# Kernel optimization log

Hardware: AMD Instinct MI355X
Metric: run time of the kernel (lower is better)

The kernel has to match this reference:

```python
import jax, jax.numpy as jnp
import numpy as np

N_NODES = 100000
N_EDGES = 1600000
IN_CH = 128
OUT_CH = 128


def setup_inputs() -> dict:
    key = jax.random.key(0)
    k1, k2, k3 = jax.random.split(key, 3)
    x = jax.random.normal(k1, (N_NODES, IN_CH), dtype=jnp.float32)
    edge_index = jax.random.randint(k2, (2, N_EDGES), 0, N_NODES, dtype=jnp.int64)
    # glorot-like init for the linear weight, stored as [in, out]
    W = jax.random.normal(k3, (IN_CH, OUT_CH), dtype=jnp.float32) * (2.0 / (IN_CH + OUT_CH)) ** 0.5
    bias = jnp.zeros((OUT_CH,), dtype=jnp.float32)
    return {"x": x, "edge_index": edge_index, "W": W, "bias": bias}


def reference(x, edge_index, W, bias):
    N = x.shape[0]
    # linear transform (bias-free, matches Linear(in, out, bias=False))
    h = x @ W  # [N, out]

    # add self loops (improved=False -> fill_value = 1.0)
    loop = jnp.arange(N, dtype=edge_index.dtype)
    src = jnp.concatenate([edge_index[0], loop])
    dst = jnp.concatenate([edge_index[1], loop])
    ew = jnp.ones(src.shape[0], dtype=h.dtype)  # edge_weight None -> ones

    # symmetric GCN normalization: deg from dst, norm = d^-1/2[src] * w * d^-1/2[dst]
    deg = jax.ops.segment_sum(ew, dst, num_segments=N)
    deg_inv_sqrt = jnp.where(deg > 0, jax.lax.rsqrt(deg), 0.0)
    w = deg_inv_sqrt[src] * ew * deg_inv_sqrt[dst]

    # spmm aggregation: out[dst] += w * h[src]
    out = jax.ops.segment_sum(h[src] * w[:, None], dst, num_segments=N)
    return out + bias
```

## Files before the change

kernel.cpp:

```cpp
#include <hip/hip_runtime.h>
#include <hip/hip_bf16.h>

constexpr int kNodes = 100000;
constexpr int kEdges = 1600000;
constexpr int kCh    = 128;
constexpr int kCap   = 32;
constexpr int kOvfCap = 8192;
constexpr int kPartSize = kNodes / 8;
constexpr int kFillBlocks = 512;
constexpr int kGemmBlocks = (kNodes + 127) / 128;

typedef __attribute__((ext_vector_type(8))) short short8;
typedef __attribute__((ext_vector_type(4))) float floatx4;
typedef __attribute__((ext_vector_type(4))) int   intx4;


__global__ __launch_bounds__(512) void k_fused(const float* __restrict__ x,
                                               const float* __restrict__ W,
                                               const int* __restrict__ srcArr,
                                               const int* __restrict__ dstArr,
                                               int* __restrict__ cnt,
                                               int* __restrict__ bucket,
                                               int* __restrict__ ovfCnt,
                                               int* __restrict__ ovfD,
                                               int* __restrict__ ovfS,
                                               __hip_bfloat16* __restrict__ hs) {
  if (blockIdx.x < kFillBlocks) {
    int part = blockIdx.x & 7;
    int bip  = blockIdx.x >> 3;
    int lo = part * kPartSize;
    const intx4* d4 = (const intx4*)dstArr;
    const intx4* s4 = (const intx4*)srcArr;
    for (int i = bip * 512 + (int)threadIdx.x; i < kEdges / 4; i += (kFillBlocks >> 3) * 512) {
      intx4 dv = __builtin_nontemporal_load(d4 + i);
      intx4 sv = __builtin_nontemporal_load(s4 + i);
      #pragma unroll
      for (int k = 0; k < 4; k++) {
        int d = dv[k];
        if ((unsigned)(d - lo) < (unsigned)kPartSize) {
          int pos = atomicAdd(&cnt[d], 1);
          if (pos < kCap) {
            bucket[(long)d * kCap + pos] = sv[k];
          } else {
            int o = atomicAdd(ovfCnt, 1);
            if (o < kOvfCap) { ovfD[o] = d; ovfS[o] = sv[k]; }
          }
        }
      }
    }
    return;
  }

  __shared__ short8 Bf[2048];
  for (int e = threadIdx.x; e < 2048; e += 512) {
    int lane = e & 63, c = (e >> 6) & 3, tt = e >> 8;
    int quad = lane >> 4, mcol = lane & 15;
    short8 v;
    #pragma unroll
    for (int j = 0; j < 8; j++) {
      __hip_bfloat16 h = __float2bfloat16(W[(c * 32 + quad * 8 + j) * kCh + tt * 16 + mcol]);
      v[j] = *(short*)&h;
    }
    Bf[e] = v;
  }
  __syncthreads();

  int wave = threadIdx.x >> 6;
  int lane = threadIdx.x & 63;
  int quad = lane >> 4;
  int mcol = lane & 15;
  int gb = blockIdx.x - kFillBlocks;
  long rowBase = ((long)gb * 8 + wave) * 16;
  if (rowBase >= kNodes) return;

  long arow = rowBase + mcol;
  if (arow >= kNodes) arow = kNodes - 1;
  const float* xp = x + arow * kCh;
  short8 afrag[4];
  #pragma unroll
  for (int c = 0; c < 4; c++) {
    const floatx4* p = (const floatx4*)(xp + c * 32 + quad * 8);
    floatx4 v0 = __builtin_nontemporal_load(p);
    floatx4 v1 = __builtin_nontemporal_load(p + 1);
    #pragma unroll
    for (int j = 0; j < 4; j++) {
      __hip_bfloat16 h0 = __float2bfloat16(v0[j]);
      __hip_bfloat16 h1 = __float2bfloat16(v1[j]);
      afrag[c][j]     = *(short*)&h0;
      afrag[c][j + 4] = *(short*)&h1;
    }
  }

  #pragma unroll
  for (int t = 0; t < 8; t++) {
    floatx4 acc = {0.f, 0.f, 0.f, 0.f};
    #pragma unroll
    for (int c = 0; c < 4; c++) {
      short8 b = Bf[(t * 4 + c) * 64 + lane];
      acc = __builtin_amdgcn_mfma_f32_16x16x32_bf16(afrag[c], b, acc, 0, 0, 0);
    }
    #pragma unroll
    for (int i = 0; i < 4; i++) {
      long r = rowBase + quad * 4 + i;
      if (r < kNodes) {
        __hip_bfloat16 h = __float2bfloat16(acc[i]);
        __builtin_nontemporal_store(*(short*)&h, (short*)hs + r * kCh + t * 16 + mcol);
      }
    }
  }
}


__global__ __launch_bounds__(256) void k_dinv(const int* __restrict__ cnt,
                                              float* __restrict__ dinv) {
  int i = blockIdx.x * 256 + threadIdx.x;
  if (i < kNodes) dinv[i] = rsqrtf((float)(cnt[i] + 1));
}


__global__ __launch_bounds__(256) void k_aggregate(const int* __restrict__ cnt,
                                                   const int* __restrict__ bucket,
                                                   const float* __restrict__ dinv,
                                                   const int* __restrict__ ovfCnt,
                                                   const int* __restrict__ ovfD,
                                                   const int* __restrict__ ovfS,
                                                   const __hip_bfloat16* __restrict__ hs,
                                                   const float* __restrict__ bias,
                                                   float* __restrict__ out) {
  int gid  = blockIdx.x * 256 + threadIdx.x;
  int node = gid >> 6;
  int lane = gid & 63;
  if (node >= kNodes) return;

  const __hip_bfloat162* hbase = (const __hip_bfloat162*)hs;

  int degRaw = cnt[node];
  float dd = dinv[node];

  float2 sf = __bfloat1622float2(hbase[(long)node * (kCh / 2) + lane]);
  float acc0 = dd * sf.x;
  float acc1 = dd * sf.y;

  int c = degRaw < kCap ? degRaw : kCap;
  const int* bkt = bucket + (long)node * kCap;

  int j = 0;
  for (; j + 7 < c; j += 8) {
    int s[8];
    #pragma unroll
    for (int u = 0; u < 8; u++) s[u] = bkt[j + u];
    float dv[8];
    #pragma unroll
    for (int u = 0; u < 8; u++) dv[u] = dinv[s[u]];
    __hip_bfloat162 v[8];
    #pragma unroll
    for (int u = 0; u < 8; u++) v[u] = hbase[(long)s[u] * (kCh / 2) + lane];
    #pragma unroll
    for (int u = 0; u < 8; u++) {
      float2 f = __bfloat1622float2(v[u]);
      acc0 = fmaf(dv[u], f.x, acc0);
      acc1 = fmaf(dv[u], f.y, acc1);
    }
  }
  for (; j < c; ++j) {
    int s = bkt[j];
    float dv = dinv[s];
    float2 f = __bfloat1622float2(hbase[(long)s * (kCh / 2) + lane]);
    acc0 = fmaf(dv, f.x, acc0);
    acc1 = fmaf(dv, f.y, acc1);
  }

  if (degRaw > kCap) {
    int n = *ovfCnt;
    if (n > kOvfCap) n = kOvfCap;
    for (int i = 0; i < n; i++) {
      if (ovfD[i] == node) {
        int s = ovfS[i];
        float2 f = __bfloat1622float2(hbase[(long)s * (kCh / 2) + lane]);
        acc0 = fmaf(dinv[s], f.x, acc0);
        acc1 = fmaf(dinv[s], f.y, acc1);
      }
    }
  }

  float2 b = ((const float2*)bias)[lane];
  float2 o;
  o.x = dd * acc0 + b.x;
  o.y = dd * acc1 + b.y;
  ((float2*)(out + (long)node * kCh))[lane] = o;
}


extern "C" void kernel_launch(void* const* d_in, const int* in_sizes, int n_in,
                              void* d_out, int out_size, void* d_ws, size_t ws_size,
                              hipStream_t stream) {
  const float* x    = (const float*)d_in[0];
  const int*   ei   = (const int*)d_in[1];
  const float* W    = (const float*)d_in[2];
  const float* bias = (const float*)d_in[3];
  float* out = (float*)d_out;

  const int* srcArr = ei;
  const int* dstArr = ei + kEdges;

  char* ws = (char*)d_ws;
  size_t off = 0;
  __hip_bfloat16* hs = (__hip_bfloat16*)(ws + off); off += (size_t)kNodes * kCh * 2;
  int*   bucket  = (int*)  (ws + off); off += (size_t)kNodes * kCap * 4;
  float* dinv    = (float*)(ws + off); off += (size_t)kNodes * 4;
  char* zbase = ws + off;
  int*   cnt     = (int*)(ws + off); off += (size_t)kNodes * 4;
  int*   ovfCnt  = (int*)(ws + off); off += 128;
  size_t zbytes = (size_t)((ws + off) - zbase);
  int*   ovfD    = (int*)(ws + off); off += (size_t)kOvfCap * 4;
  int*   ovfS    = (int*)(ws + off); off += (size_t)kOvfCap * 4;

  (void)hipMemsetAsync(zbase, 0, zbytes, stream);

  k_fused<<<kFillBlocks + kGemmBlocks, 512, 0, stream>>>(x, W, srcArr, dstArr, cnt, bucket,
                                                         ovfCnt, ovfD, ovfS, hs);

  k_dinv<<<(kNodes + 255) / 256, 256, 0, stream>>>(cnt, dinv);

  long aggThreads = (long)kNodes * 64;
  int gAgg = (int)((aggThreads + 255) / 256);
  k_aggregate<<<gAgg, 256, 0, stream>>>(cnt, bucket, dinv, ovfCnt, ovfD, ovfS,
                                        hs, bias, out);
}
```

Baseline: 265.4 us.

## Replace global per-node atomic bucketing with two-level LDS binning of edges

Edge bucketing now bins edges by destination into 256-node bins using shared-memory atomics per block, writing packed (local dst, src) entries to per-block segments instead of doing global atomics on per-node counters. Degree is rebuilt per bin via an LDS histogram, and aggregation blocks gather their 64 nodes' edges from all segments into LDS buckets before gathering features. This removes global atomic contention and the large memset, but each aggregation block must scan all 128 segment slots for its bin, so segment data is read several times. Overflow handling becomes more involved.

```diff
diff --git a/kernel.cpp b/kernel.cpp
--- a/kernel.cpp
+++ b/kernel.cpp
@@ -5,10 +5,15 @@
 constexpr int kEdges = 1600000;
 constexpr int kCh    = 128;
 constexpr int kCap   = 32;
-constexpr int kOvfCap = 8192;
-constexpr int kPartSize = kNodes / 8;
-constexpr int kFillBlocks = 512;
+constexpr int kOvfCap = 4096;
+constexpr int kLOvf  = 512;
+constexpr int kBinShift = 8;
+constexpr int kBinSize  = 1 << kBinShift;
+constexpr int kBins  = (kNodes + kBinSize - 1) >> kBinShift;
+constexpr int kABlocks = 128;
+constexpr int kChunkCap = 64;
 constexpr int kGemmBlocks = (kNodes + 127) / 128;
+constexpr int kAggBlocks = (kNodes + 63) / 64;
 
 typedef __attribute__((ext_vector_type(8))) short short8;
 typedef __attribute__((ext_vector_type(4))) float floatx4;
@@ -19,34 +24,39 @@
                                                const float* __restrict__ W,
                                                const int* __restrict__ srcArr,
                                                const int* __restrict__ dstArr,
-                                               int* __restrict__ cnt,
-                                               int* __restrict__ bucket,
+                                               unsigned* __restrict__ segs,
+                                               int* __restrict__ segCnt,
                                                int* __restrict__ ovfCnt,
                                                int* __restrict__ ovfD,
                                                int* __restrict__ ovfS,
                                                __hip_bfloat16* __restrict__ hs) {
-  if (blockIdx.x < kFillBlocks) {
-    int part = blockIdx.x & 7;
-    int bip  = blockIdx.x >> 3;
-    int lo = part * kPartSize;
+  if (blockIdx.x < kABlocks) {
+    __shared__ int lcnt[kBins];
+    for (int i = threadIdx.x; i < kBins; i += 512) lcnt[i] = 0;
+    __syncthreads();
     const intx4* d4 = (const intx4*)dstArr;
     const intx4* s4 = (const intx4*)srcArr;
-    for (int i = bip * 512 + (int)threadIdx.x; i < kEdges / 4; i += (kFillBlocks >> 3) * 512) {
+    unsigned* myseg = segs + (long)blockIdx.x * kBins * kChunkCap;
+    for (int i = blockIdx.x * 512 + (int)threadIdx.x; i < kEdges / 4; i += kABlocks * 512) {
       intx4 dv = __builtin_nontemporal_load(d4 + i);
       intx4 sv = __builtin_nontemporal_load(s4 + i);
       #pragma unroll
       for (int k = 0; k < 4; k++) {
-        int d = dv[k];
-        if ((unsigned)(d - lo) < (unsigned)kPartSize) {
-          int pos = atomicAdd(&cnt[d], 1);
-          if (pos < kCap) {
-            bucket[(long)d * kCap + pos] = sv[k];
-          } else {
-            int o = atomicAdd(ovfCnt, 1);
-            if (o < kOvfCap) { ovfD[o] = d; ovfS[o] = sv[k]; }
-          }
+        int d = dv[k], s = sv[k];
+        int bin = d >> kBinShift;
+        int pos = atomicAdd(&lcnt[bin], 1);
+        if (pos < kChunkCap) {
+          myseg[bin * kChunkCap + pos] = ((unsigned)(d & (kBinSize - 1)) << 17) | (unsigned)s;
+        } else {
+          int o = atomicAdd(ovfCnt, 1);
+          if (o < kOvfCap) { ovfD[o] = d; ovfS[o] = s; }
         }
       }
+    }
+    __syncthreads();
+    for (int i = threadIdx.x; i < kBins; i += 512) {
+      int c = lcnt[i];
+      segCnt[blockIdx.x * kBins + i] = c < kChunkCap ? c : kChunkCap;
     }
     return;
   }
@@ -69,7 +79,7 @@
   int lane = threadIdx.x & 63;
   int quad = lane >> 4;
   int mcol = lane & 15;
-  int gb = blockIdx.x - kFillBlocks;
+  int gb = blockIdx.x - kABlocks;
   long rowBase = ((long)gb * 8 + wave) * 16;
   if (rowBase >= kNodes) return;
 
@@ -111,83 +121,145 @@
 }
 
 
-__global__ __launch_bounds__(256) void k_dinv(const int* __restrict__ cnt,
+__global__ __launch_bounds__(256) void k_dinv(const unsigned* __restrict__ segs,
+                                              const int* __restrict__ segCnt,
+                                              const int* __restrict__ ovfCnt,
+                                              const int* __restrict__ ovfD,
                                               float* __restrict__ dinv) {
-  int i = blockIdx.x * 256 + threadIdx.x;
-  if (i < kNodes) dinv[i] = rsqrtf((float)(cnt[i] + 1));
-}
-
-
-__global__ __launch_bounds__(256) void k_aggregate(const int* __restrict__ cnt,
-                                                   const int* __restrict__ bucket,
-                                                   const float* __restrict__ dinv,
-                                                   const int* __restrict__ ovfCnt,
-                                                   const int* __restrict__ ovfD,
-                                                   const int* __restrict__ ovfS,
-                                                   const __hip_bfloat16* __restrict__ hs,
-                                                   const float* __restrict__ bias,
-                                                   float* __restrict__ out) {
-  int gid  = blockIdx.x * 256 + threadIdx.x;
-  int node = gid >> 6;
-  int lane = gid & 63;
-  if (node >= kNodes) return;
-
+  __shared__ int lsn[kABlocks];
+  __shared__ int hist[kBinSize];
+  int bin = blockIdx.x;
+  for (int i = threadIdx.x; i < kABlocks; i += 256) lsn[i] = segCnt[i * kBins + bin];
+  for (int i = threadIdx.x; i < kBinSize; i += 256) hist[i] = 0;
+  __syncthreads();
+
+  for (int slot = threadIdx.x; slot < kABlocks * kChunkCap; slot += 256) {
+    int blk = slot >> 6, pos = slot & (kChunkCap - 1);
+    if (pos < lsn[blk]) {
+      unsigned e = segs[((long)blk * kBins + bin) * kChunkCap + pos];
+      atomicAdd(&hist[e >> 17], 1);
+    }
+  }
+  int n = *ovfCnt; if (n > kOvfCap) n = kOvfCap;
+  for (int i = threadIdx.x; i < n; i += 256) {
+    int d = ovfD[i];
+    if ((d >> kBinShift) == bin) atomicAdd(&hist[d & (kBinSize - 1)], 1);
+  }
+  __syncthreads();
+  int base = bin << kBinShift;
+  for (int i = threadIdx.x; i < kBinSize; i += 256) {
+    int node = base + i;
+    if (node < kNodes) dinv[node] = rsqrtf((float)(hist[i] + 1));
+  }
+}
+
+
+__global__ __launch_bounds__(512) void k_agg(const unsigned* __restrict__ segs,
+                                             const int* __restrict__ segCnt,
+                                             const int* __restrict__ ovfCnt,
+                                             const int* __restrict__ ovfD,
+                                             const int* __restrict__ ovfS,
+                                             const float* __restrict__ dinv,
+                                             const __hip_bfloat16* __restrict__ hs,
+                                             const float* __restrict__ bias,
+                                             float* __restrict__ out) {
+  __shared__ int lsn[kABlocks];
+  __shared__ int lcnt[64];
+  __shared__ __align__(16) int lbkt[64][kCap];
+  __shared__ unsigned lovf[kLOvf];
+  __shared__ int lovfn;
+
+  int base = blockIdx.x * 64;
+  int bin  = base >> kBinShift;
+  int q    = (base >> 6) & 3;
+
+  for (int i = threadIdx.x; i < kABlocks; i += 512) lsn[i] = segCnt[i * kBins + bin];
+  for (int i = threadIdx.x; i < 64; i += 512) lcnt[i] = 0;
+  if (threadIdx.x == 0) lovfn = 0;
+  __syncthreads();
+
+  for (int slot = threadIdx.x; slot < kABlocks * kChunkCap; slot += 512) {
+    int blk = slot >> 6, pos = slot & (kChunkCap - 1);
+    if (pos < lsn[blk]) {
+      unsigned e = segs[((long)blk * kBins + bin) * kChunkCap + pos];
+      int r = (int)(e >> 17) - q * 64;
+      if ((unsigned)r < 64u) {
+        int p = atomicAdd(&lcnt[r], 1);
+        if (p < kCap) lbkt[r][p] = (int)(e & 0x1ffff);
+        else { int o = atomicAdd(&lovfn, 1); if (o < kLOvf) lovf[o] = ((unsigned)r << 17) | (e & 0x1ffff); }
+      }
+    }
+  }
+  {
+    int n = *ovfCnt; if (n > kOvfCap) n = kOvfCap;
+    for (int i = threadIdx.x; i < n; i += 512) {
+      int d = ovfD[i];
+      if ((d >> 6) == blockIdx.x) {
+        int r = d & 63;
+        int p = atomicAdd(&lcnt[r], 1);
+        if (p < kCap) lbkt[r][p] = ovfS[i];
+        else { int o = atomicAdd(&lovfn, 1); if (o < kLOvf) lovf[o] = ((unsigned)r << 17) | (unsigned)ovfS[i]; }
+      }
+    }
+  }
+  __syncthreads();
+
+  int wave = threadIdx.x >> 6;
+  int lane = threadIdx.x & 63;
   const __hip_bfloat162* hbase = (const __hip_bfloat162*)hs;
-
-  int degRaw = cnt[node];
-  float dd = dinv[node];
-
-  float2 sf = __bfloat1622float2(hbase[(long)node * (kCh / 2) + lane]);
-  float acc0 = dd * sf.x;
-  float acc1 = dd * sf.y;
-
-  int c = degRaw < kCap ? degRaw : kCap;
-  const int* bkt = bucket + (long)node * kCap;
-
-  int j = 0;
-  for (; j + 7 < c; j += 8) {
-    int s[8];
-    #pragma unroll
-    for (int u = 0; u < 8; u++) s[u] = bkt[j + u];
-    float dv[8];
-    #pragma unroll
-    for (int u = 0; u < 8; u++) dv[u] = dinv[s[u]];
-    __hip_bfloat162 v[8];
-    #pragma unroll
-    for (int u = 0; u < 8; u++) v[u] = hbase[(long)s[u] * (kCh / 2) + lane];
-    #pragma unroll
-    for (int u = 0; u < 8; u++) {
-      float2 f = __bfloat1622float2(v[u]);
-      acc0 = fmaf(dv[u], f.x, acc0);
-      acc1 = fmaf(dv[u], f.y, acc1);
-    }
-  }
-  for (; j < c; ++j) {
-    int s = bkt[j];
-    float dv = dinv[s];
-    float2 f = __bfloat1622float2(hbase[(long)s * (kCh / 2) + lane]);
-    acc0 = fmaf(dv, f.x, acc0);
-    acc1 = fmaf(dv, f.y, acc1);
-  }
-
-  if (degRaw > kCap) {
-    int n = *ovfCnt;
-    if (n > kOvfCap) n = kOvfCap;
-    for (int i = 0; i < n; i++) {
-      if (ovfD[i] == node) {
-        int s = ovfS[i];
+  int novf = lovfn; if (novf > kLOvf) novf = kLOvf;
+
+  for (int t = 0; t < 8; t++) {
+    int r = wave * 8 + t;
+    int node = base + r;
+    if (node >= kNodes) break;
+
+    float dd = dinv[node];
+    float2 sf = __bfloat1622float2(hbase[(long)node * (kCh / 2) + lane]);
+    float acc0 = dd * sf.x;
+    float acc1 = dd * sf.y;
+
+    int c = lcnt[r]; if (c > kCap) c = kCap;
+    int j = 0;
+    for (; j + 7 < c; j += 8) {
+      int s[8];
+      #pragma unroll
+      for (int u = 0; u < 8; u++) s[u] = lbkt[r][j + u];
+      float dv[8];
+      #pragma unroll
+      for (int u = 0; u < 8; u++) dv[u] = dinv[s[u]];
+      __hip_bfloat162 v[8];
+      #pragma unroll
+      for (int u = 0; u < 8; u++) v[u] = hbase[(long)s[u] * (kCh / 2) + lane];
+      #pragma unroll
+      for (int u = 0; u < 8; u++) {
+        float2 f = __bfloat1622float2(v[u]);
+        acc0 = fmaf(dv[u], f.x, acc0);
+        acc1 = fmaf(dv[u], f.y, acc1);
+      }
+    }
+    for (; j < c; ++j) {
+      int s = lbkt[r][j];
+      float dv = dinv[s];
+      float2 f = __bfloat1622float2(hbase[(long)s * (kCh / 2) + lane]);
+      acc0 = fmaf(dv, f.x, acc0);
+      acc1 = fmaf(dv, f.y, acc1);
+    }
+    for (int i = 0; i < novf; i++) {
+      if ((int)(lovf[i] >> 17) == r) {
+        int s = (int)(lovf[i] & 0x1ffff);
         float2 f = __bfloat1622float2(hbase[(long)s * (kCh / 2) + lane]);
         acc0 = fmaf(dinv[s], f.x, acc0);
         acc1 = fmaf(dinv[s], f.y, acc1);
       }
     }
-  }
-
-  float2 b = ((const float2*)bias)[lane];
-  float2 o;
-  o.x = dd * acc0 + b.x;
-  o.y = dd * acc1 + b.y;
-  ((float2*)(out + (long)node * kCh))[lane] = o;
+
+    float2 b = ((const float2*)bias)[lane];
+    float2 o;
+    o.x = dd * acc0 + b.x;
+    o.y = dd * acc1 + b.y;
+    ((float2*)(out + (long)node * kCh))[lane] = o;
+  }
 }
 
 
@@ -206,24 +278,20 @@
   char* ws = (char*)d_ws;
   size_t off = 0;
   __hip_bfloat16* hs = (__hip_bfloat16*)(ws + off); off += (size_t)kNodes * kCh * 2;
-  int*   bucket  = (int*)  (ws + off); off += (size_t)kNodes * kCap * 4;
-  float* dinv    = (float*)(ws + off); off += (size_t)kNodes * 4;
-  char* zbase = ws + off;
-  int*   cnt     = (int*)(ws + off); off += (size_t)kNodes * 4;
-  int*   ovfCnt  = (int*)(ws + off); off += 128;
-  size_t zbytes = (size_t)((ws + off) - zbase);
-  int*   ovfD    = (int*)(ws + off); off += (size_t)kOvfCap * 4;
-  int*   ovfS    = (int*)(ws + off); off += (size_t)kOvfCap * 4;
-
-  (void)hipMemsetAsync(zbase, 0, zbytes, stream);
-
-  k_fused<<<kFillBlocks + kGemmBlocks, 512, 0, stream>>>(x, W, srcArr, dstArr, cnt, bucket,
-                                                         ovfCnt, ovfD, ovfS, hs);
-
-  k_dinv<<<(kNodes + 255) / 256, 256, 0, stream>>>(cnt, dinv);
-
-  long aggThreads = (long)kNodes * 64;
-  int gAgg = (int)((aggThreads + 255) / 256);
-  k_aggregate<<<gAgg, 256, 0, stream>>>(cnt, bucket, dinv, ovfCnt, ovfD, ovfS,
-                                        hs, bias, out);
-}
+  unsigned* segs = (unsigned*)(ws + off); off += (size_t)kABlocks * kBins * kChunkCap * 4;
+  float* dinv    = (float*)   (ws + off); off += (size_t)kNodes * 4;
+  int*   segCnt  = (int*)     (ws + off); off += (size_t)kABlocks * kBins * 4;
+  int*   ovfCnt  = (int*)     (ws + off); off += 64;
+  int*   ovfD    = (int*)     (ws + off); off += (size_t)kOvfCap * 4;
+  int*   ovfS    = (int*)     (ws + off); off += (size_t)kOvfCap * 4;
+
+  (void)hipMemsetAsync(ovfCnt, 0, 64, stream);
+
+  k_fused<<<kABlocks + kGemmBlocks, 512, 0, stream>>>(x, W, srcArr, dstArr,
+                                                      segs, segCnt, ovfCnt, ovfD, ovfS, hs);
+
+  k_dinv<<<kBins, 256, 0, stream>>>(segs, segCnt, ovfCnt, ovfD, dinv);
+
+  k_agg<<<kAggBlocks, 512, 0, stream>>>(segs, segCnt, ovfCnt, ovfD, ovfS,
+                                        dinv, hs, bias, out);
+}
```

Result: faster. 240.8 us (-9.3%).
